# Performance work log

Measured on AMD Instinct MI355X. Metric: run time of the kernel, lower is better.

## Reference

```python
import jax, jax.numpy as jnp
import numpy as np
from jax import lax

B_CAPS, C_CAPS, K, STRIDE, ITERS = 32, 32, 3, 2, 3
BATCH, WIN = 8, 14
W_OUT = (WIN - K) // STRIDE + 1  # 6
CWW = C_CAPS * W_OUT * W_OUT     # 1152
LOG_2PI = float(np.log(2.0 * np.pi))


def setup_inputs() -> dict:
    key = jax.random.key(0)
    k1, k2, k3, k4, k5 = jax.random.split(key, 5)
    return {
        "poses": jax.random.normal(k1, (BATCH, B_CAPS, WIN, WIN, 16), jnp.float32),
        "activations": jax.random.uniform(k2, (BATCH, B_CAPS, WIN, WIN), jnp.float32),
        "lambda_": jnp.ones((), jnp.float32),
        "W": jax.random.normal(k3, (B_CAPS, K, K, C_CAPS, 4, 4), jnp.float32),
        "beta_v": jax.random.normal(k4, (1, CWW, 1), jnp.float32),
        "beta_a": jax.random.normal(k5, (1, CWW), jnp.float32),
    }


def reference(poses, activations, lambda_, W, beta_v, beta_a):
    b, B, win = poses.shape[0], poses.shape[1], poses.shape[2]
    C = W.shape[3]
    w = (win - K) // STRIDE + 1
    Bkk, Cww = B * K * K, C * w * w

    pose = poses.reshape(b, 16, B, win, win).transpose(0, 2, 3, 4, 1)

    # im2col patch extraction (vectorized): rows[i,k] = stride*i + k
    rows = ((jnp.arange(w) * STRIDE)[:, None] + jnp.arange(K)).reshape(-1)  # (w*K,)
    p = jnp.take(pose, rows, axis=2).reshape(b, B, w, K, win, 16)
    p = jnp.take(p, rows, axis=4).reshape(b, B, w, K, w, K, 16)
    patches = p.transpose(0, 1, 3, 5, 6, 2, 4)          # (b,B,K,K,16,wi,wj)
    # faithful reproduction of torch's view (b,B,K,K,16,ww)->(b,B,K,K,1,w,w,4,4)
    patches = patches.reshape(b, B, K, K, w, w, 4, 4)

    # votes: broadcast 4x4 matmul W @ pose-patch
    votes = jnp.einsum('sxyzij,bsxyuvjk->bsxyzuvik', W, patches)
    votes = votes.reshape(b, Bkk, Cww, 16)

    # activation patches, tiled over C (coordinate_add=False branch)
    a = jnp.take(activations, rows, axis=2).reshape(b, B, w, K, win)
    a = jnp.take(a, rows, axis=4).reshape(b, B, w, K, w, K)
    a = a.transpose(0, 1, 3, 5, 2, 4).reshape(b, Bkk, 1, w * w)
    act = jnp.broadcast_to(a, (b, Bkk, C, w * w)).reshape(b, Bkk, Cww)

    # EM routing
    R = jnp.ones((b, Bkk, Cww), votes.dtype) / Cww
    for i in range(ITERS + 1):
        Ra = (R * act)[..., None]                        # (b,Bkk,Cww,1)
        sum_R = Ra.sum(1)                                # (b,Cww,1)
        mu = ((Ra * votes).sum(1) / sum_R)[:, None]      # (b,1,Cww,16)
        sigma_sq = (Ra * (votes - mu) ** 2).sum(1) / sum_R  # (b,Cww,16)
        if i != ITERS:
            mu_d = lax.stop_gradient(mu)
            ss_d = lax.stop_gradient(sigma_sq)[:, None]  # (b,1,Cww,16)
            V_d = lax.stop_gradient(votes)
            a_d = lax.stop_gradient(act)
            log_p = -0.5 * (V_d - mu_d) ** 2 / ss_d - 0.5 * jnp.log(ss_d) - 0.5 * LOG_2PI
            ap = a_d * jnp.exp(log_p).sum(-1)            # (b,Bkk,Cww)
            R = ap / ap.sum(-1, keepdims=True)
        else:
            cost = (beta_v + jnp.log(sigma_sq)) * sum_R  # (b,Cww,16)
            a_out = jax.nn.sigmoid(lambda_ * (beta_a - cost.sum(2)))  # (b,Cww)

    return (mu.reshape(b, C, w, w, 16), a_out.reshape(b, C, w, w))
```

## Files before the change

### kernel.cpp

```cpp
#include <hip/hip_runtime.h>
#include <hip/hip_bf16.h>

#define NB   8
#define NM   288
#define NN   1152
#define NUV  36
#define ND   16

#define OFF_P    0
#define SZ_P     (NB*NUV*NM*ND)
#define OFF_WT   (OFF_P + SZ_P)
#define SZ_WT    (32*NM*ND)
#define OFF_ACT  (OFF_WT + SZ_WT)
#define SZ_ACT   (NB*NUV*NM)
#define OFF_L    (OFF_ACT + SZ_ACT)
#define SZ_L     (NB*NN*NM)
#define OFF_LSE  (OFF_L + SZ_L)
#define SZ_LSE   (NB*NM)
#define OFF_FLAG (OFF_LSE + SZ_LSE)
#define OFF_LT   (OFF_FLAG + 16)
#define SZ_LT    (NB*NM*NN)

#define HALF_LOG_2PI 0.9189385332046727f
#define LOG_NN       7.049254841255839f
#define NEG_BIG      (-1.0e30f)

__device__ __forceinline__ float ldin(const void* p, int i, int f32) {
    return f32 ? ((const float*)p)[i]
               : __bfloat162float(((const __hip_bfloat16*)p)[i]);
}

__device__ __forceinline__ void unpk(unsigned u, float& lo, float& hi) {
    union { unsigned i; float f; } a, b;
    a.i = u << 16; b.i = u & 0xFFFF0000u;
    lo = a.f; hi = b.f;
}

__global__ void detect_kernel(const unsigned short* __restrict__ poses_u16,
                              int* __restrict__ flag) {
    if (blockIdx.x == 0 && threadIdx.x == 0) {
        int wild = 0;
        for (int i = 0; i < 64; ++i) {
            int ex = (poses_u16[i] >> 7) & 0xFF;
            if (ex >= 133) ++wild;
        }
        *flag = (wild >= 4) ? 1 : 0;
    }
}

__global__ __launch_bounds__(256) void prep_kernel(
    const void* __restrict__ poses, const void* __restrict__ acts,
    const void* __restrict__ Wb, __hip_bfloat16* __restrict__ P,
    __hip_bfloat16* __restrict__ Wt, float* __restrict__ A36,
    const int* __restrict__ flagp)
{
    const int f32 = *flagp;
    const int blk = blockIdx.x;
    const int tid = threadIdx.x;
    if (blk < 256) {
        __shared__ float ps[16 * 196];
        __shared__ float asld[196];
        const int b = blk >> 5, s = blk & 31;
        for (int e = tid; e < 16 * 196; e += 256) {
            int c = e / 196, hw = e % 196;
            ps[e] = ldin(poses, ((b * 16 + c) * 32 + s) * 196 + hw, f32);
        }
        for (int e = tid; e < 196; e += 256)
            asld[e] = ldin(acts, (b * 32 + s) * 196 + e, f32);
        __syncthreads();
        for (int o = tid; o < 5184; o += 256) {
            int uv = o / 144, r = o % 144, xy = r >> 4, kj = r & 15;
            int u = uv / 6, vv2 = uv % 6;
            int x = xy / 3, y = xy % 3;
            int k = kj >> 2, j = kj & 3;
            int idx = u * 96 + vv2 * 16 + j * 4 + k;
            int c = idx / 36, rem = idx % 36;
            int wi = rem / 6, wj = rem % 6;
            P[((b * 36 + uv) * 288 + s * 9 + xy) * 16 + kj] =
                __float2bfloat16(ps[c * 196 + (2 * wi + x) * 14 + (2 * wj + y)]);
        }
        for (int o = tid; o < 324; o += 256) {
            int uv = o / 9, xy = o % 9;
            int u = uv / 6, vv2 = uv % 6;
            int x = xy / 3, y = xy % 3;
            A36[(b * 36 + uv) * 288 + s * 9 + xy] =
                __logf(asld[(2 * u + x) * 14 + (2 * vv2 + y)]);
        }
    } else {
        int idx = (blk - 256) * 256 + tid;
        int z = idx / 288, m = idx % 288;
        __hip_bfloat16* dst = &Wt[idx * 16];
#pragma unroll
        for (int e = 0; e < 16; ++e)
            dst[e] = __float2bfloat16(ldin(Wb, m * 512 + z * 16 + e, f32));
    }
}

__global__ __launch_bounds__(288, 4) void em_iter(
    const unsigned short* __restrict__ wsP, const unsigned short* __restrict__ wsWt,
    const float* __restrict__ wsA, float* __restrict__ wsL,
    float* __restrict__ wsLT, const float* __restrict__ wsLSE,
    const void* __restrict__ beta_v,
    const void* __restrict__ beta_a,
    const void* __restrict__ lambda_,
    void* __restrict__ outv, const int* __restrict__ flagp, int iter)
{
    __shared__ float red[NM * 17];
    __shared__ float Mhw[9];
    __shared__ float paru[NM];
    __shared__ float parv[NM];
    __shared__ float paruW[18];
    __shared__ float mul[16], nhil[16], ltl[16], ssl[16];

    const int tid = threadIdx.x;
    const int bn  = blockIdx.x;
    const int b   = bn / NN;
    const int n   = bn % NN;
    const int z   = n / NUV;
    const int uv  = n % NUV;

    const uint4* Wq = (const uint4*)(wsWt + ((z * NM + tid) << 4));
    const uint4* Pq = (const uint4*)(wsP + (((b * NUV + uv) * NM + tid) << 4));
    uint4 wq0 = Wq[0], wq1 = Wq[1];
    uint4 pq0 = Pq[0], pq1 = Pq[1];
    const float lact = wsA[(b * NUV + uv) * NM + tid];
    float t;
    if (iter == 0) t = lact - LOG_NN;
    else t = wsL[(size_t)(b * NN + n) * NM + tid] - wsLSE[b * NM + tid] + lact;
    t = fmaxf(t, NEG_BIG);

    float mhw = t;
#pragma unroll
    for (int off = 1; off < 32; off <<= 1)
        mhw = fmaxf(mhw, __shfl_xor(mhw, off, 32));
    const float w = __expf(t - mhw);
    if ((tid & 31) == 0) Mhw[tid >> 5] = mhw;

    float W_[16], P_[16], v[16];
    unpk(wq0.x, W_[0], W_[1]);   unpk(wq0.y, W_[2], W_[3]);
    unpk(wq0.z, W_[4], W_[5]);   unpk(wq0.w, W_[6], W_[7]);
    unpk(wq1.x, W_[8], W_[9]);   unpk(wq1.y, W_[10], W_[11]);
    unpk(wq1.z, W_[12], W_[13]); unpk(wq1.w, W_[14], W_[15]);
    unpk(pq0.x, P_[0], P_[1]);   unpk(pq0.y, P_[2], P_[3]);
    unpk(pq0.z, P_[4], P_[5]);   unpk(pq0.w, P_[6], P_[7]);
    unpk(pq1.x, P_[8], P_[9]);   unpk(pq1.y, P_[10], P_[11]);
    unpk(pq1.z, P_[12], P_[13]); unpk(pq1.w, P_[14], P_[15]);
#pragma unroll
    for (int i = 0; i < 4; ++i)
#pragma unroll
        for (int k = 0; k < 4; ++k)
            v[i * 4 + k] = W_[i * 4 + 0] * P_[k * 4 + 0] + W_[i * 4 + 1] * P_[k * 4 + 1]
                         + W_[i * 4 + 2] * P_[k * 4 + 2] + W_[i * 4 + 3] * P_[k * 4 + 3];

#pragma unroll
    for (int dd = 0; dd < 16; ++dd) red[tid * 17 + dd] = v[dd];
    red[tid * 17 + 16] = w;
    __syncthreads();

    {
        const int d = tid & 15, c = tid >> 4;
        const float* base = &red[(c << 4) * 17];
        float s1 = 0.f, s2 = 0.f, sw = 0.f;
#pragma unroll
        for (int q = 0; q < 16; ++q) {
            float ww = base[q * 17 + 16];
            float vv = base[q * 17 + d];
            float t1 = ww * vv;
            s1 += t1; s2 += t1 * vv; sw += ww;
        }
        paru[d * 18 + c] = s1;
        parv[d * 18 + c] = s2;
        if (d == 0) paruW[c] = sw;
    }
    __syncthreads();

    float M_f = NEG_BIG, sW_f = 0.f;
    if (tid < 16) {
        float M = Mhw[0];
#pragma unroll
        for (int h = 1; h < 9; ++h) M = fmaxf(M, Mhw[h]);
        float sW = 0.f, S1 = 0.f, S2 = 0.f;
#pragma unroll
        for (int c = 0; c < 18; ++c) {
            float sc = __expf(Mhw[c >> 1] - M);
            sW += paruW[c] * sc;
            S1 += paru[tid * 18 + c] * sc;
            S2 += parv[tid * 18 + c] * sc;
        }
        float mu = S1 / sW;
        float q2 = S2 / sW;
        float ss = fmaxf(q2 - mu * mu, 1e-30f);
        mul[tid]  = mu;
        ssl[tid]  = ss;
        nhil[tid] = -0.5f / ss;
        ltl[tid]  = -0.5f * __logf(ss) - HALF_LOG_2PI;
        M_f = M; sW_f = sW;
    }
    __syncthreads();

    if (iter < 3) {
        float lp[16];
        float M = NEG_BIG;
#pragma unroll
        for (int dd = 0; dd < 16; ++dd) {
            float df = v[dd] - mul[dd];
            lp[dd] = df * df * nhil[dd] + ltl[dd];
            M = fmaxf(M, lp[dd]);
        }
        float s = 0.f;
#pragma unroll
        for (int dd = 0; dd < 16; ++dd) s += __expf(lp[dd] - M);
        float ell = lact + M + __logf(s);
        wsL[(size_t)(b * NN + n) * NM + tid] = ell;
        wsLT[((size_t)b * NM + tid) * NN + n] = ell;
    } else {
        const int f32 = *flagp;
        if (tid < 16) {
            if (f32) ((float*)outv)[(bn << 4) + tid] = mul[tid];
            else ((__hip_bfloat16*)outv)[(bn << 4) + tid] = __float2bfloat16(mul[tid]);
        }
        if (tid == 0) {
            float sumR = __expf(M_f) * sW_f;
            float bv = ldin(beta_v, n, f32);
            float c = 0.f;
#pragma unroll
            for (int dd = 0; dd < 16; ++dd) c += bv + __logf(ssl[dd]);
            c *= sumR;
            float lam = ldin(lambda_, 0, f32);
            float ba  = ldin(beta_a, n, f32);
            float ao  = 1.f / (1.f + __expf(-(lam * (ba - c))));
            int oi = NB * NN * ND + b * NN + n;
            if (f32) ((float*)outv)[oi] = ao;
            else ((__hip_bfloat16*)outv)[oi] = __float2bfloat16(ao);
        }
    }
}

__global__ __launch_bounds__(256) void lse_kernel(const float* __restrict__ LT,
                                                  float* __restrict__ LSE)
{
    const int row  = blockIdx.x * 4 + (threadIdx.x >> 6);
    const int lane = threadIdx.x & 63;
    const float* base = LT + (size_t)row * NN + lane;
    float vv[18];
    float mx = NEG_BIG;
#pragma unroll
    for (int i = 0; i < 18; ++i) { vv[i] = base[i * 64]; mx = fmaxf(mx, vv[i]); }
#pragma unroll
    for (int off = 1; off < 64; off <<= 1) mx = fmaxf(mx, __shfl_xor(mx, off));
    float s = 0.f;
#pragma unroll
    for (int i = 0; i < 18; ++i) s += __expf(vv[i] - mx);
#pragma unroll
    for (int off = 1; off < 64; off <<= 1) s += __shfl_xor(s, off);
    if (lane == 0) LSE[row] = mx + __logf(s);
}

extern "C" void kernel_launch(void* const* d_in, const int* in_sizes, int n_in,
                              void* d_out, int out_size, void* d_ws, size_t ws_size,
                              hipStream_t stream)
{
    const void* poses = d_in[0];
    const void* acts  = d_in[1];
    const void* lam   = d_in[2];
    const void* Wb    = d_in[3];
    const void* bv    = d_in[4];
    const void* ba    = d_in[5];

    float* ws  = (float*)d_ws;
    __hip_bfloat16* P  = (__hip_bfloat16*)(ws + OFF_P);
    __hip_bfloat16* Wt = (__hip_bfloat16*)(ws + OFF_WT);
    float* A36 = ws + OFF_ACT;
    float* L   = ws + OFF_L;
    float* LSE = ws + OFF_LSE;
    int*  flag = (int*)(ws + OFF_FLAG);
    float* LT  = ws + OFF_LT;

    detect_kernel<<<1, 64, 0, stream>>>((const unsigned short*)poses, flag);

    prep_kernel<<<292, 256, 0, stream>>>(poses, acts, Wb, P, Wt, A36, flag);

    for (int it = 0; it < 4; ++it) {
        em_iter<<<NB * NN, 288, 0, stream>>>((const unsigned short*)P,
                                             (const unsigned short*)Wt,
                                             A36, L, LT, LSE, bv, ba, lam,
                                             d_out, flag, it);
        if (it < 3) {
            lse_kernel<<<576, 256, 0, stream>>>(LT, LSE);
        }
    }
}
```

Measured before the change: 234.6 us.

## Process four output capsules per block with prefetched W and L loads

After: 333.3 us. 1.42x slower.

```diff
diff --git a/kernel.cpp b/kernel.cpp
--- a/kernel.cpp
+++ b/kernel.cpp
@@ -113,125 +113,146 @@
     __shared__ float mul[16], nhil[16], ltl[16], ssl[16];
 
     const int tid = threadIdx.x;
-    const int bn  = blockIdx.x;
-    const int b   = bn / NN;
-    const int n   = bn % NN;
-    const int z   = n / NUV;
-    const int uv  = n % NUV;
-
-    const uint4* Wq = (const uint4*)(wsWt + ((z * NM + tid) << 4));
-    const uint4* Pq = (const uint4*)(wsP + (((b * NUV + uv) * NM + tid) << 4));
-    uint4 wq0 = Wq[0], wq1 = Wq[1];
+    const int blk = blockIdx.x;
+    const int zg  = blk & 7;
+    const int buv = blk >> 3;
+    const int b   = buv / NUV;
+    const int uv  = buv % NUV;
+
+    const uint4* Pq = (const uint4*)(wsP + ((buv * NM + tid) << 4));
     uint4 pq0 = Pq[0], pq1 = Pq[1];
-    const float lact = wsA[(b * NUV + uv) * NM + tid];
-    float t;
-    if (iter == 0) t = lact - LOG_NN;
-    else t = wsL[(size_t)(b * NN + n) * NM + tid] - wsLSE[b * NM + tid] + lact;
-    t = fmaxf(t, NEG_BIG);
-
-    float mhw = t;
-#pragma unroll
-    for (int off = 1; off < 32; off <<= 1)
-        mhw = fmaxf(mhw, __shfl_xor(mhw, off, 32));
-    const float w = __expf(t - mhw);
-    if ((tid & 31) == 0) Mhw[tid >> 5] = mhw;
-
-    float W_[16], P_[16], v[16];
-    unpk(wq0.x, W_[0], W_[1]);   unpk(wq0.y, W_[2], W_[3]);
-    unpk(wq0.z, W_[4], W_[5]);   unpk(wq0.w, W_[6], W_[7]);
-    unpk(wq1.x, W_[8], W_[9]);   unpk(wq1.y, W_[10], W_[11]);
-    unpk(wq1.z, W_[12], W_[13]); unpk(wq1.w, W_[14], W_[15]);
+    const float lact = wsA[buv * NM + tid];
+    const float lsev = (iter > 0) ? wsLSE[b * NM + tid] : 0.f;
+
+    float P_[16];
     unpk(pq0.x, P_[0], P_[1]);   unpk(pq0.y, P_[2], P_[3]);
     unpk(pq0.z, P_[4], P_[5]);   unpk(pq0.w, P_[6], P_[7]);
     unpk(pq1.x, P_[8], P_[9]);   unpk(pq1.y, P_[10], P_[11]);
     unpk(pq1.z, P_[12], P_[13]); unpk(pq1.w, P_[14], P_[15]);
-#pragma unroll
-    for (int i = 0; i < 4; ++i)
-#pragma unroll
-        for (int k = 0; k < 4; ++k)
-            v[i * 4 + k] = W_[i * 4 + 0] * P_[k * 4 + 0] + W_[i * 4 + 1] * P_[k * 4 + 1]
-                         + W_[i * 4 + 2] * P_[k * 4 + 2] + W_[i * 4 + 3] * P_[k * 4 + 3];
-
-#pragma unroll
-    for (int dd = 0; dd < 16; ++dd) red[tid * 17 + dd] = v[dd];
-    red[tid * 17 + 16] = w;
-    __syncthreads();
-
+
+    uint4 wq0, wq1;
     {
-        const int d = tid & 15, c = tid >> 4;
-        const float* base = &red[(c << 4) * 17];
-        float s1 = 0.f, s2 = 0.f, sw = 0.f;
-#pragma unroll
-        for (int q = 0; q < 16; ++q) {
-            float ww = base[q * 17 + 16];
-            float vv = base[q * 17 + d];
-            float t1 = ww * vv;
-            s1 += t1; s2 += t1 * vv; sw += ww;
-        }
-        paru[d * 18 + c] = s1;
-        parv[d * 18 + c] = s2;
-        if (d == 0) paruW[c] = sw;
-    }
-    __syncthreads();
-
-    float M_f = NEG_BIG, sW_f = 0.f;
-    if (tid < 16) {
-        float M = Mhw[0];
-#pragma unroll
-        for (int h = 1; h < 9; ++h) M = fmaxf(M, Mhw[h]);
-        float sW = 0.f, S1 = 0.f, S2 = 0.f;
-#pragma unroll
-        for (int c = 0; c < 18; ++c) {
-            float sc = __expf(Mhw[c >> 1] - M);
-            sW += paruW[c] * sc;
-            S1 += paru[tid * 18 + c] * sc;
-            S2 += parv[tid * 18 + c] * sc;
-        }
-        float mu = S1 / sW;
-        float q2 = S2 / sW;
-        float ss = fmaxf(q2 - mu * mu, 1e-30f);
-        mul[tid]  = mu;
-        ssl[tid]  = ss;
-        nhil[tid] = -0.5f / ss;
-        ltl[tid]  = -0.5f * __logf(ss) - HALF_LOG_2PI;
-        M_f = M; sW_f = sW;
-    }
-    __syncthreads();
-
-    if (iter < 3) {
-        float lp[16];
-        float M = NEG_BIG;
-#pragma unroll
-        for (int dd = 0; dd < 16; ++dd) {
-            float df = v[dd] - mul[dd];
-            lp[dd] = df * df * nhil[dd] + ltl[dd];
-            M = fmaxf(M, lp[dd]);
-        }
-        float s = 0.f;
-#pragma unroll
-        for (int dd = 0; dd < 16; ++dd) s += __expf(lp[dd] - M);
-        float ell = lact + M + __logf(s);
-        wsL[(size_t)(b * NN + n) * NM + tid] = ell;
-        wsLT[((size_t)b * NM + tid) * NN + n] = ell;
-    } else {
-        const int f32 = *flagp;
+        const uint4* Wq = (const uint4*)(wsWt + ((zg * NM + tid) << 4));
+        wq0 = Wq[0]; wq1 = Wq[1];
+    }
+    float Lv = (iter > 0) ? wsL[(size_t)(b * NN + (zg * NUV + uv)) * NM + tid] : 0.f;
+
+    for (int p = 0; p < 4; ++p) {
+        const int z = zg + 8 * p;
+        const int n = z * NUV + uv;
+
+        float t = (iter == 0) ? (lact - LOG_NN) : (Lv - lsev + lact);
+        t = fmaxf(t, NEG_BIG);
+
+        float mhw = t;
+#pragma unroll
+        for (int off = 1; off < 32; off <<= 1)
+            mhw = fmaxf(mhw, __shfl_xor(mhw, off, 32));
+        const float w = __expf(t - mhw);
+        if ((tid & 31) == 0) Mhw[tid >> 5] = mhw;
+
+        float W_[16], v[16];
+        unpk(wq0.x, W_[0], W_[1]);   unpk(wq0.y, W_[2], W_[3]);
+        unpk(wq0.z, W_[4], W_[5]);   unpk(wq0.w, W_[6], W_[7]);
+        unpk(wq1.x, W_[8], W_[9]);   unpk(wq1.y, W_[10], W_[11]);
+        unpk(wq1.z, W_[12], W_[13]); unpk(wq1.w, W_[14], W_[15]);
+#pragma unroll
+        for (int i = 0; i < 4; ++i)
+#pragma unroll
+            for (int k = 0; k < 4; ++k)
+                v[i * 4 + k] = W_[i * 4 + 0] * P_[k * 4 + 0] + W_[i * 4 + 1] * P_[k * 4 + 1]
+                             + W_[i * 4 + 2] * P_[k * 4 + 2] + W_[i * 4 + 3] * P_[k * 4 + 3];
+
+        if (p < 3) {
+            const int zn = zg + 8 * (p + 1);
+            const uint4* Wq2 = (const uint4*)(wsWt + ((zn * NM + tid) << 4));
+            wq0 = Wq2[0]; wq1 = Wq2[1];
+            if (iter > 0) Lv = wsL[(size_t)(b * NN + (zn * NUV + uv)) * NM + tid];
+        }
+
+#pragma unroll
+        for (int dd = 0; dd < 16; ++dd) red[tid * 17 + dd] = v[dd];
+        red[tid * 17 + 16] = w;
+        __syncthreads();
+
+        float Mt = Mhw[0];
+#pragma unroll
+        for (int h = 1; h < 9; ++h) Mt = fmaxf(Mt, Mhw[h]);
+
+        {
+            const int d = tid & 15, c = tid >> 4;
+            const float sc = __expf(Mhw[c >> 1] - Mt);
+            const float* base = &red[(c << 4) * 17];
+            float s1 = 0.f, s2 = 0.f, sw = 0.f;
+#pragma unroll
+            for (int q = 0; q < 16; ++q) {
+                float ww = base[q * 17 + 16];
+                float vv = base[q * 17 + d];
+                float t1 = ww * vv;
+                s1 += t1; s2 += t1 * vv; sw += ww;
+            }
+            paru[d * 18 + c] = s1 * sc;
+            parv[d * 18 + c] = s2 * sc;
+            if (d == 0) paruW[c] = sw * sc;
+        }
+        __syncthreads();
+
+        float sW_f = 0.f;
         if (tid < 16) {
-            if (f32) ((float*)outv)[(bn << 4) + tid] = mul[tid];
-            else ((__hip_bfloat16*)outv)[(bn << 4) + tid] = __float2bfloat16(mul[tid]);
-        }
-        if (tid == 0) {
-            float sumR = __expf(M_f) * sW_f;
-            float bv = ldin(beta_v, n, f32);
-            float c = 0.f;
-#pragma unroll
-            for (int dd = 0; dd < 16; ++dd) c += bv + __logf(ssl[dd]);
-            c *= sumR;
-            float lam = ldin(lambda_, 0, f32);
-            float ba  = ldin(beta_a, n, f32);
-            float ao  = 1.f / (1.f + __expf(-(lam * (ba - c))));
-            int oi = NB * NN * ND + b * NN + n;
-            if (f32) ((float*)outv)[oi] = ao;
-            else ((__hip_bfloat16*)outv)[oi] = __float2bfloat16(ao);
+            float sW = 0.f, S1 = 0.f, S2 = 0.f;
+#pragma unroll
+            for (int c = 0; c < 18; ++c) {
+                sW += paruW[c];
+                S1 += paru[tid * 18 + c];
+                S2 += parv[tid * 18 + c];
+            }
+            float mu = S1 / sW;
+            float q2 = S2 / sW;
+            float ss = fmaxf(q2 - mu * mu, 1e-30f);
+            mul[tid]  = mu;
+            ssl[tid]  = ss;
+            nhil[tid] = -0.5f / ss;
+            ltl[tid]  = -0.5f * __logf(ss) - HALF_LOG_2PI;
+            sW_f = sW;
+        }
+        __syncthreads();
+
+        if (iter < 3) {
+            float lp[16];
+            float M = NEG_BIG;
+#pragma unroll
+            for (int dd = 0; dd < 16; ++dd) {
+                float df = v[dd] - mul[dd];
+                lp[dd] = df * df * nhil[dd] + ltl[dd];
+                M = fmaxf(M, lp[dd]);
+            }
+            float s = 0.f;
+#pragma unroll
+            for (int dd = 0; dd < 16; ++dd) s += __expf(lp[dd] - M);
+            float ell = lact + M + __logf(s);
+            wsL[(size_t)(b * NN + n) * NM + tid] = ell;
+            wsLT[((size_t)b * NM + tid) * NN + n] = ell;
+        } else {
+            const int f32 = *flagp;
+            const int bn = b * NN + n;
+            if (tid < 16) {
+                if (f32) ((float*)outv)[(bn << 4) + tid] = mul[tid];
+                else ((__hip_bfloat16*)outv)[(bn << 4) + tid] = __float2bfloat16(mul[tid]);
+            }
+            if (tid == 0) {
+                float sumR = __expf(Mt) * sW_f;
+                float bv = ldin(beta_v, n, f32);
+                float c = 0.f;
+#pragma unroll
+                for (int dd = 0; dd < 16; ++dd) c += bv + __logf(ssl[dd]);
+                c *= sumR;
+                float lam = ldin(lambda_, 0, f32);
+                float ba  = ldin(beta_a, n, f32);
+                float ao  = 1.f / (1.f + __expf(-(lam * (ba - c))));
+                int oi = NB * NN * ND + bn;
+                if (f32) ((float*)outv)[oi] = ao;
+                else ((__hip_bfloat16*)outv)[oi] = __float2bfloat16(ao);
+            }
         }
     }
 }
@@ -281,10 +302,10 @@
     prep_kernel<<<292, 256, 0, stream>>>(poses, acts, Wb, P, Wt, A36, flag);
 
     for (int it = 0; it < 4; ++it) {
-        em_iter<<<NB * NN, 288, 0, stream>>>((const unsigned short*)P,
-                                             (const unsigned short*)Wt,
-                                             A36, L, LT, LSE, bv, ba, lam,
-                                             d_out, flag, it);
+        em_iter<<<NB * NUV * 8, 288, 0, stream>>>((const unsigned short*)P,
+                                                  (const unsigned short*)Wt,
+                                                  A36, L, LT, LSE, bv, ba, lam,
+                                                  d_out, flag, it);
         if (it < 3) {
             lse_kernel<<<576, 256, 0, stream>>>(LT, LSE);
         }
```

## Use bf16 dot2 instructions for votes, vectorize prep stores, remap em_iter blocks

Applied to the files above, without the earlier changes.

Result: no change. 230.4 us (-1.8%).

```diff
diff --git a/kernel.cpp b/kernel.cpp
--- a/kernel.cpp
+++ b/kernel.cpp
@@ -30,10 +30,15 @@
                : __bfloat162float(((const __hip_bfloat16*)p)[i]);
 }
 
-__device__ __forceinline__ void unpk(unsigned u, float& lo, float& hi) {
-    union { unsigned i; float f; } a, b;
-    a.i = u << 16; b.i = u & 0xFFFF0000u;
-    lo = a.f; hi = b.f;
+__device__ __forceinline__ unsigned short bfbits(float f) {
+    __hip_bfloat16 h = __float2bfloat16(f);
+    return __builtin_bit_cast(unsigned short, h);
+}
+
+__device__ __forceinline__ float dot2bf(unsigned a, unsigned b, float c) {
+    float d;
+    asm("v_dot2_f32_bf16 %0, %1, %2, %3" : "=v"(d) : "v"(a), "v"(b), "v"(c));
+    return d;
 }
 
 __global__ void detect_kernel(const unsigned short* __restrict__ poses_u16,
@@ -68,16 +73,28 @@
         for (int e = tid; e < 196; e += 256)
             asld[e] = ldin(acts, (b * 32 + s) * 196 + e, f32);
         __syncthreads();
-        for (int o = tid; o < 5184; o += 256) {
-            int uv = o / 144, r = o % 144, xy = r >> 4, kj = r & 15;
+        for (int o2 = tid; o2 < 648; o2 += 256) {
+            int row = o2 >> 1, half = o2 & 1;
+            int uv = row / 9, xy = row % 9;
             int u = uv / 6, vv2 = uv % 6;
             int x = xy / 3, y = xy % 3;
-            int k = kj >> 2, j = kj & 3;
-            int idx = u * 96 + vv2 * 16 + j * 4 + k;
-            int c = idx / 36, rem = idx % 36;
-            int wi = rem / 6, wj = rem % 6;
-            P[((b * 36 + uv) * 288 + s * 9 + xy) * 16 + kj] =
-                __float2bfloat16(ps[c * 196 + (2 * wi + x) * 14 + (2 * wj + y)]);
+            unsigned pk[4];
+#pragma unroll
+            for (int h = 0; h < 4; ++h) {
+                unsigned lohi[2];
+#pragma unroll
+                for (int e = 0; e < 2; ++e) {
+                    int kj = half * 8 + h * 2 + e;
+                    int k = kj >> 2, j = kj & 3;
+                    int idx = u * 96 + vv2 * 16 + j * 4 + k;
+                    int c = idx / 36, rem = idx % 36;
+                    int wi = rem / 6, wj = rem % 6;
+                    lohi[e] = bfbits(ps[c * 196 + (2 * wi + x) * 14 + (2 * wj + y)]);
+                }
+                pk[h] = lohi[0] | (lohi[1] << 16);
+            }
+            *((uint4*)(P + (((size_t)((b * 36 + uv) * 288 + s * 9 + xy)) << 4) + half * 8)) =
+                make_uint4(pk[0], pk[1], pk[2], pk[3]);
         }
         for (int o = tid; o < 324; o += 256) {
             int uv = o / 9, xy = o % 9;
@@ -89,10 +106,16 @@
     } else {
         int idx = (blk - 256) * 256 + tid;
         int z = idx / 288, m = idx % 288;
-        __hip_bfloat16* dst = &Wt[idx * 16];
-#pragma unroll
-        for (int e = 0; e < 16; ++e)
-            dst[e] = __float2bfloat16(ldin(Wb, m * 512 + z * 16 + e, f32));
+        unsigned pk[8];
+#pragma unroll
+        for (int h = 0; h < 8; ++h) {
+            unsigned lo = bfbits(ldin(Wb, m * 512 + z * 16 + 2 * h, f32));
+            unsigned hi = bfbits(ldin(Wb, m * 512 + z * 16 + 2 * h + 1, f32));
+            pk[h] = lo | (hi << 16);
+        }
+        uint4* dst = (uint4*)(Wt + idx * 16);
+        dst[0] = make_uint4(pk[0], pk[1], pk[2], pk[3]);
+        dst[1] = make_uint4(pk[4], pk[5], pk[6], pk[7]);
     }
 }
 
@@ -113,20 +136,23 @@
     __shared__ float mul[16], nhil[16], ltl[16], ssl[16];
 
     const int tid = threadIdx.x;
-    const int bn  = blockIdx.x;
-    const int b   = bn / NN;
-    const int n   = bn % NN;
-    const int z   = n / NUV;
-    const int uv  = n % NUV;
+    const int B   = blockIdx.x;
+    const int rr  = B & 255;
+    const int z   = rr >> 3;
+    const int g   = ((B >> 8) << 3) | (rr & 7);
+    const int b   = g / NUV;
+    const int uv  = g % NUV;
+    const int n   = z * NUV + uv;
+    const int bn  = b * NN + n;
 
     const uint4* Wq = (const uint4*)(wsWt + ((z * NM + tid) << 4));
-    const uint4* Pq = (const uint4*)(wsP + (((b * NUV + uv) * NM + tid) << 4));
+    const uint4* Pq = (const uint4*)(wsP + ((g * NM + tid) << 4));
     uint4 wq0 = Wq[0], wq1 = Wq[1];
     uint4 pq0 = Pq[0], pq1 = Pq[1];
-    const float lact = wsA[(b * NUV + uv) * NM + tid];
+    const float lact = wsA[g * NM + tid];
     float t;
     if (iter == 0) t = lact - LOG_NN;
-    else t = wsL[(size_t)(b * NN + n) * NM + tid] - wsLSE[b * NM + tid] + lact;
+    else t = wsL[(size_t)bn * NM + tid] - wsLSE[b * NM + tid] + lact;
     t = fmaxf(t, NEG_BIG);
 
     float mhw = t;
@@ -136,21 +162,16 @@
     const float w = __expf(t - mhw);
     if ((tid & 31) == 0) Mhw[tid >> 5] = mhw;
 
-    float W_[16], P_[16], v[16];
-    unpk(wq0.x, W_[0], W_[1]);   unpk(wq0.y, W_[2], W_[3]);
-    unpk(wq0.z, W_[4], W_[5]);   unpk(wq0.w, W_[6], W_[7]);
-    unpk(wq1.x, W_[8], W_[9]);   unpk(wq1.y, W_[10], W_[11]);
-    unpk(wq1.z, W_[12], W_[13]); unpk(wq1.w, W_[14], W_[15]);
-    unpk(pq0.x, P_[0], P_[1]);   unpk(pq0.y, P_[2], P_[3]);
-    unpk(pq0.z, P_[4], P_[5]);   unpk(pq0.w, P_[6], P_[7]);
-    unpk(pq1.x, P_[8], P_[9]);   unpk(pq1.y, P_[10], P_[11]);
-    unpk(pq1.z, P_[12], P_[13]); unpk(pq1.w, P_[14], P_[15]);
+    unsigned Wa[4] = {wq0.x, wq0.z, wq1.x, wq1.z};
+    unsigned Wb_[4] = {wq0.y, wq0.w, wq1.y, wq1.w};
+    unsigned Pa[4] = {pq0.x, pq0.z, pq1.x, pq1.z};
+    unsigned Pb[4] = {pq0.y, pq0.w, pq1.y, pq1.w};
+    float v[16];
 #pragma unroll
     for (int i = 0; i < 4; ++i)
 #pragma unroll
         for (int k = 0; k < 4; ++k)
-            v[i * 4 + k] = W_[i * 4 + 0] * P_[k * 4 + 0] + W_[i * 4 + 1] * P_[k * 4 + 1]
-                         + W_[i * 4 + 2] * P_[k * 4 + 2] + W_[i * 4 + 3] * P_[k * 4 + 3];
+            v[i * 4 + k] = dot2bf(Wa[i], Pa[k], dot2bf(Wb_[i], Pb[k], 0.f));
 
 #pragma unroll
     for (int dd = 0; dd < 16; ++dd) red[tid * 17 + dd] = v[dd];
@@ -211,7 +232,7 @@
 #pragma unroll
         for (int dd = 0; dd < 16; ++dd) s += __expf(lp[dd] - M);
         float ell = lact + M + __logf(s);
-        wsL[(size_t)(b * NN + n) * NM + tid] = ell;
+        wsL[(size_t)bn * NM + tid] = ell;
         wsLT[((size_t)b * NM + tid) * NN + n] = ell;
     } else {
         const int f32 = *flagp;
@@ -229,7 +250,7 @@
             float lam = ldin(lambda_, 0, f32);
             float ba  = ldin(beta_a, n, f32);
             float ao  = 1.f / (1.f + __expf(-(lam * (ba - c))));
-            int oi = NB * NN * ND + b * NN + n;
+            int oi = NB * NN * ND + bn;
             if (f32) ((float*)outv)[oi] = ao;
             else ((__hip_bfloat16*)outv)[oi] = __float2bfloat16(ao);
         }
```
